# Kernel tuning notes

Hardware: AMD Instinct MI355X
Metric: run time of the kernel (lower is better)

Reference implementation:

```python
import jax, jax.numpy as jnp
import numpy as np

B, S, L = 2, 512, 12
DIM, H, HD = 1024, 16, 64
MAX_SEQ, DFF = 1024, 4096
VOCAB, CODE_HEADS = 2048, 7
THETA, EPS = 10000.0, 1e-5


def _rope_tables():
    inv_freq = 1.0 / (THETA ** (jnp.arange(0, HD, 2, dtype=jnp.float32) / HD))
    t = jnp.arange(MAX_SEQ, dtype=jnp.float32)
    freqs = t[:, None] * inv_freq[None, :]          # [MAX, HD/2]
    emb = jnp.concatenate([freqs, freqs], axis=-1)  # [MAX, HD]
    return jnp.cos(emb), jnp.sin(emb)


def _rotate_half(x):
    x1, x2 = x[..., : HD // 2], x[..., HD // 2:]
    return jnp.concatenate([-x2, x1], axis=-1)


def _rms(x, w):
    v = jnp.mean(x * x, axis=-1, keepdims=True)
    return x * jax.lax.rsqrt(v + EPS) * w


def setup_inputs() -> dict:
    key = jax.random.key(0)
    ks = jax.random.split(key, 12)
    std = 0.02
    rn = lambda k, shp: jax.random.normal(k, shp, jnp.float32) * std
    fused_input2 = jax.random.normal(ks[0], (B, S, DIM), jnp.float32)
    primary_hidden = jax.random.normal(ks[1], (B, S, DIM), jnp.float32)
    position_ids = jnp.broadcast_to(jnp.arange(S), (B, S))
    cache_position = jnp.arange(S)
    # causal additive mask over the full cache length
    allowed = jnp.arange(MAX_SEQ)[None, :] <= cache_position[:, None]  # [S, MAX]
    attn_mask = jnp.broadcast_to(
        jnp.where(allowed, 0.0, -1e9)[None, None], (B, 1, S, MAX_SEQ)
    ).astype(jnp.float32)
    return {
        'fused_input2': fused_input2,
        'primary_hidden': primary_hidden,
        'attn_mask': attn_mask,
        'w_bridge': rn(ks[2], (2 * DIM, DIM)),
        'ln1_w': jnp.ones((L, DIM), jnp.float32),
        'wq': rn(ks[3], (L, DIM, DIM)),
        'wk': rn(ks[4], (L, DIM, DIM)),
        'wv': rn(ks[5], (L, DIM, DIM)),
        'wo': rn(ks[6], (L, DIM, DIM)),
        'ln2_w': jnp.ones((L, DIM), jnp.float32),
        'w_gate': rn(ks[7], (L, DIM, DFF)),
        'w_up': rn(ks[8], (L, DIM, DFF)),
        'w_down': rn(ks[9], (L, DFF, DIM)),
        'norm_w': jnp.ones((DIM,), jnp.float32),
        'w_out': rn(ks[10], (CODE_HEADS, DIM, VOCAB)),
        'position_ids': position_ids,
        'cache_position': cache_position,
    }


def reference(fused_input2, primary_hidden, attn_mask, w_bridge, ln1_w, wq, wk, wv,
              wo, ln2_w, w_gate, w_up, w_down, norm_w, w_out,
              position_ids, cache_position):
    rope_cos, rope_sin = _rope_tables()
    cos = rope_cos[position_ids][:, None]  # [B,1,S,HD]
    sin = rope_sin[position_ids][:, None]
    scale = 1.0 / np.sqrt(HD).astype(np.float32)
    h = jnp.concatenate([fused_input2, primary_hidden], axis=-1) @ w_bridge
    for i in range(L):
        x = _rms(h, ln1_w[i])
        q = (x @ wq[i]).reshape(B, S, H, HD).transpose(0, 2, 1, 3)
        k = (x @ wk[i]).reshape(B, S, H, HD).transpose(0, 2, 1, 3)
        v = (x @ wv[i]).reshape(B, S, H, HD).transpose(0, 2, 1, 3)
        q = q * cos + _rotate_half(q) * sin
        k = k * cos + _rotate_half(k) * sin
        # scatter-style KV-cache write at cache_position
        kc = jnp.zeros((B, H, MAX_SEQ, HD), x.dtype).at[:, :, cache_position, :].set(k)
        vc = jnp.zeros((B, H, MAX_SEQ, HD), x.dtype).at[:, :, cache_position, :].set(v)
        s = jnp.einsum('bhsd,bhtd->bhst', q, kc) * scale + attn_mask
        p = jax.nn.softmax(s.astype(jnp.float32), axis=-1).astype(x.dtype)
        o = jnp.einsum('bhst,bhtd->bhsd', p, vc).transpose(0, 2, 1, 3).reshape(B, S, DIM)
        h = h + o @ wo[i]
        r = h
        x = _rms(h, ln2_w[i])
        h = r + (jax.nn.silu(x @ w_gate[i]) * (x @ w_up[i])) @ w_down[i]
    h = _rms(h, norm_w)
    # [B, code_depth-1, S, VOCAB]
    return jnp.einsum('bsd,kdv->bksv', h, w_out).astype(jnp.float32)
```

## Files before the change

### kernel.cpp

```cpp
#include <hip/hip_runtime.h>

#define NB    2
#define SEQ   512
#define NL    12
#define DIM   1024
#define NH    16
#define HD    64
#define DFF   4096
#define VOCAB 2048
#define CHD   7

typedef __attribute__((ext_vector_type(4))) float f32x4;
typedef __attribute__((ext_vector_type(8))) short s16x8;
typedef __attribute__((ext_vector_type(4))) unsigned short u16x4;
typedef __attribute__((ext_vector_type(8))) unsigned short u16x8;

__device__ __forceinline__ unsigned short f2bf(float f) {
    unsigned u = __builtin_bit_cast(unsigned, f);
    u += 0x7fffu + ((u >> 16) & 1u);
    return (unsigned short)(u >> 16);
}

__device__ __forceinline__ void gl2lds16(const void* g, void* l) {
    __builtin_amdgcn_global_load_lds(
        (const __attribute__((address_space(1))) void*)g,
        (__attribute__((address_space(3))) void*)l, 16, 0, 0);
}

template<bool ATOMIC>
__global__ __launch_bounds__(256)
void gemm_bf(const unsigned short* __restrict__ A,
             const unsigned short* __restrict__ B0,
             const unsigned short* __restrict__ B1,
             const unsigned short* __restrict__ B2,
             float* __restrict__ C, int K, int lda, int ldbT, int ldc,
             int rhi, long sBz, long sCz, int kchunk, int ksplit)
{
    __shared__ unsigned short sm[4][8192];

    const int tid = threadIdx.x;
    const int z   = blockIdx.z;
    const int wsel = z / ksplit, kz = z - wsel * ksplit;
    const int m0  = blockIdx.y * 128;
    const int n0  = blockIdx.x * 128;
    const int koff = kz * kchunk;

    const unsigned short* Ap = A + koff;
    const unsigned short* Bp = sBz ? (B0 + (long)wsel * sBz)
                                   : (wsel == 0 ? B0 : (wsel == 1 ? B1 : B2));
    Bp += koff;
    float* Cp = C + (long)wsel * sCz;

    const int w = tid >> 6, l = tid & 63;
    const int lrow = l & 15, lhi = l >> 4;
    const int wm = (w >> 1) * 64, wn = (w & 1) * 64;

    int rowS[4], colS[4];
    #pragma unroll
    for (int i = 0; i < 4; ++i) {
        const int c = w * 256 + i * 64 + l;
        rowS[i] = c >> 3;
        colS[i] = (((c & 7) ^ ((c >> 3) & 7)) << 3);
    }

    f32x4 acc[4][4] = {};

    auto STAGE = [&](int d, int k0) {
        unsigned short* Ab = &sm[d * 2][0];
        unsigned short* Bb = &sm[d * 2 + 1][0];
        #pragma unroll
        for (int i = 0; i < 4; ++i) {
            const int ub = (w * 256 + i * 64) * 8;
            gl2lds16(Ap + (long)(m0 + rowS[i]) * lda + k0 + colS[i], Ab + ub);
            gl2lds16(Bp + (long)(n0 + rowS[i]) * ldbT + k0 + colS[i], Bb + ub);
        }
    };
    auto COMPUTE = [&](int d) {
        const char* Ab = (const char*)&sm[d * 2][0];
        const char* Bb = (const char*)&sm[d * 2 + 1][0];
        #pragma unroll
        for (int ks = 0; ks < 2; ++ks) {
            s16x8 af[4], bf[4];
            #pragma unroll
            for (int i = 0; i < 4; ++i) {
                const int r = wm + i * 16 + lrow;
                af[i] = __builtin_bit_cast(s16x8, *reinterpret_cast<const u16x8*>(
                    Ab + r * 128 + (((ks * 4 + lhi) ^ (r & 7)) << 4)));
            }
            #pragma unroll
            for (int j = 0; j < 4; ++j) {
                const int r = wn + j * 16 + lrow;
                bf[j] = __builtin_bit_cast(s16x8, *reinterpret_cast<const u16x8*>(
                    Bb + r * 128 + (((ks * 4 + lhi) ^ (r & 7)) << 4)));
            }
            #pragma unroll
            for (int i = 0; i < 4; ++i)
                #pragma unroll
                for (int j = 0; j < 4; ++j)
                    acc[i][j] = __builtin_amdgcn_mfma_f32_16x16x32_bf16(af[i], bf[j], acc[i][j], 0, 0, 0);
        }
    };

    STAGE(0, 0);
    __syncthreads();
    int cur = 0;
    for (int k0 = 0; k0 < K; k0 += 64) {
        if (k0 + 64 < K) STAGE(cur ^ 1, k0 + 64);
        COMPUTE(cur);
        __syncthreads();
        cur ^= 1;
    }

    #pragma unroll
    for (int i = 0; i < 4; ++i) {
        const int r0 = m0 + wm + i * 16 + lhi * 4;
        #pragma unroll
        for (int j = 0; j < 4; ++j) {
            const int c = n0 + wn + j * 16 + lrow;
            #pragma unroll
            for (int e = 0; e < 4; ++e) {
                const int r = r0 + e;
                const long idx = (long)(r >> 9) * rhi + (long)(r & 511) * ldc + c;
                if (ATOMIC) atomicAdd(&Cp[idx], acc[i][j][e]);
                else        Cp[idx] = acc[i][j][e];
            }
        }
    }
}

__global__ __launch_bounds__(256)
void gemm_gu(const unsigned short* __restrict__ A,
             const unsigned short* __restrict__ Bg0,
             const unsigned short* __restrict__ Bu0,
             unsigned short* __restrict__ GU, int K, int lda, int ldbT)
{
    __shared__ unsigned short sm[32768];
    char* const lds = (char*)sm;

    const int tid = threadIdx.x;
    const int m0  = blockIdx.y * 128;
    const int n0  = blockIdx.x * 64;

    const unsigned short* Bg = Bg0 + (long)n0 * ldbT;
    const unsigned short* Bu = Bu0 + (long)n0 * ldbT;

    const int w = tid >> 6, l = tid & 63;
    const int lrow = l & 15, lhi = l >> 4;
    const int wm = (w >> 1) * 64, wn = (w & 1) * 32;

    int rowA[4], colA[4];
    #pragma unroll
    for (int i = 0; i < 4; ++i) {
        const int c = w * 256 + i * 64 + l;
        rowA[i] = c >> 3;
        colA[i] = (((c & 7) ^ ((c >> 3) & 7)) << 3);
    }
    int rowB[2], colB[2];
    #pragma unroll
    for (int i = 0; i < 2; ++i) {
        const int c = w * 128 + i * 64 + l;
        rowB[i] = c >> 3;
        colB[i] = (((c & 7) ^ ((c >> 3) & 7)) << 3);
    }

    f32x4 accg[4][2] = {};
    f32x4 accu[4][2] = {};

    auto STAGE = [&](int d, int k0) {
        char* Ab  = lds + d * 16384;
        char* Bgb = lds + 32768 + d * 8192;
        char* Bub = lds + 49152 + d * 8192;
        #pragma unroll
        for (int i = 0; i < 4; ++i) {
            const int ub = (w * 256 + i * 64) * 16;
            gl2lds16(A + (long)(m0 + rowA[i]) * lda + k0 + colA[i], Ab + ub);
        }
        #pragma unroll
        for (int i = 0; i < 2; ++i) {
            const int ub = (w * 128 + i * 64) * 16;
            gl2lds16(Bg + (long)rowB[i] * ldbT + k0 + colB[i], Bgb + ub);
            gl2lds16(Bu + (long)rowB[i] * ldbT + k0 + colB[i], Bub + ub);
        }
    };
    auto COMPUTE = [&](int d) {
        const char* Ab  = lds + d * 16384;
        const char* Bgb = lds + 32768 + d * 8192;
        const char* Bub = lds + 49152 + d * 8192;
        #pragma unroll
        for (int ks = 0; ks < 2; ++ks) {
            s16x8 af[4], bg[2], bu[2];
            #pragma unroll
            for (int i = 0; i < 4; ++i) {
                const int r = wm + i * 16 + lrow;
                af[i] = __builtin_bit_cast(s16x8, *reinterpret_cast<const u16x8*>(
                    Ab + r * 128 + (((ks * 4 + lhi) ^ (r & 7)) << 4)));
            }
            #pragma unroll
            for (int j = 0; j < 2; ++j) {
                const int r = wn + j * 16 + lrow;
                const int off = r * 128 + (((ks * 4 + lhi) ^ (r & 7)) << 4);
                bg[j] = __builtin_bit_cast(s16x8, *reinterpret_cast<const u16x8*>(Bgb + off));
                bu[j] = __builtin_bit_cast(s16x8, *reinterpret_cast<const u16x8*>(Bub + off));
            }
            #pragma unroll
            for (int i = 0; i < 4; ++i)
                #pragma unroll
                for (int j = 0; j < 2; ++j) {
                    accg[i][j] = __builtin_amdgcn_mfma_f32_16x16x32_bf16(af[i], bg[j], accg[i][j], 0, 0, 0);
                    accu[i][j] = __builtin_amdgcn_mfma_f32_16x16x32_bf16(af[i], bu[j], accu[i][j], 0, 0, 0);
                }
        }
    };

    STAGE(0, 0);
    __syncthreads();
    int cur = 0;
    for (int k0 = 0; k0 < K; k0 += 64) {
        if (k0 + 64 < K) STAGE(cur ^ 1, k0 + 64);
        COMPUTE(cur);
        __syncthreads();
        cur ^= 1;
    }

    #pragma unroll
    for (int i = 0; i < 4; ++i) {
        const int r0 = m0 + wm + i * 16 + lhi * 4;
        #pragma unroll
        for (int j = 0; j < 2; ++j) {
            const int c = n0 + wn + j * 16 + lrow;
            #pragma unroll
            for (int e = 0; e < 4; ++e) {
                const float gx = accg[i][j][e];
                const float ux = accu[i][j][e];
                const float val = gx / (1.0f + __expf(-gx)) * ux;
                GU[(long)(r0 + e) * DFF + c] = f2bf(val);
            }
        }
    }
}

__global__ __launch_bounds__(256)
void tconv_kernel(const float* __restrict__ src, unsigned short* __restrict__ dst,
                  int R, int Cn, long sS, long sD)
{
    __shared__ float tile[64][65];
    const int c0 = blockIdx.x * 64, r0 = blockIdx.y * 64;
    const float* s = src + (long)blockIdx.z * sS;
    unsigned short* d = dst + (long)blockIdx.z * sD;
    const int tid = threadIdx.x;
    #pragma unroll
    for (int it = 0; it < 4; ++it) {
        const int idx = tid + it * 256;
        const int r = idx >> 4, c4 = (idx & 15) * 4;
        f32x4 v = *reinterpret_cast<const f32x4*>(&s[(long)(r0 + r) * Cn + c0 + c4]);
        tile[r][c4] = v[0]; tile[r][c4+1] = v[1]; tile[r][c4+2] = v[2]; tile[r][c4+3] = v[3];
    }
    __syncthreads();
    #pragma unroll
    for (int it = 0; it < 4; ++it) {
        const int idx = tid + it * 256;
        const int n = idx >> 4, r4 = (idx & 15) * 4;
        u16x4 o = { f2bf(tile[r4][n]), f2bf(tile[r4+1][n]),
                    f2bf(tile[r4+2][n]), f2bf(tile[r4+3][n]) };
        *reinterpret_cast<u16x4*>(&d[(long)(c0 + n) * R + r0 + r4]) = o;
    }
}

__global__ __launch_bounds__(256)
void ropetab_kernel(float* __restrict__ tc, float* __restrict__ ts)
{
    const int idx = blockIdx.x * 256 + threadIdx.x;
    const int pos = idx >> 5, i = idx & 31;
    const float invf = powf(10000.0f, -(float)i * (1.0f / 32.0f));
    const float ang = (float)pos * invf;
    tc[idx] = cosf(ang);
    ts[idx] = sinf(ang);
}

template<bool BF>
__global__ __launch_bounds__(256)
void concat_kernel(const float* __restrict__ a, const float* __restrict__ b,
                   void* __restrict__ outv)
{
    const long i = ((long)blockIdx.x * 256 + threadIdx.x) * 4;
    const int row = (int)(i >> 11), col = (int)(i & 2047);
    const float* src = (col < DIM) ? &a[(long)row * DIM + col]
                                   : &b[(long)row * DIM + col - DIM];
    f32x4 v = *reinterpret_cast<const f32x4*>(src);
    if (BF) {
        u16x4 o = { f2bf(v[0]), f2bf(v[1]), f2bf(v[2]), f2bf(v[3]) };
        *reinterpret_cast<u16x4*>((unsigned short*)outv + i) = o;
    } else {
        *reinterpret_cast<f32x4*>((float*)outv + i) = v;
    }
}

template<bool BF>
__global__ __launch_bounds__(256)
void rms_kernel(const float* __restrict__ in, const float* __restrict__ w,
                void* __restrict__ outv)
{
    __shared__ float red[4];
    const int row = blockIdx.x, tid = threadIdx.x;
    const long base = (long)row * DIM + tid * 4;
    f32x4 v = *reinterpret_cast<const f32x4*>(&in[base]);
    float ss = v[0]*v[0] + v[1]*v[1] + v[2]*v[2] + v[3]*v[3];
    for (int off = 32; off; off >>= 1) ss += __shfl_down(ss, off);
    if ((tid & 63) == 0) red[tid >> 6] = ss;
    __syncthreads();
    float s = red[0] + red[1] + red[2] + red[3];
    float r = 1.0f / sqrtf(s * (1.0f / DIM) + 1e-5f);
    f32x4 wv = *reinterpret_cast<const f32x4*>(&w[tid * 4]);
    f32x4 o = { v[0]*r*wv[0], v[1]*r*wv[1], v[2]*r*wv[2], v[3]*r*wv[3] };
    if (BF) {
        u16x4 ob = { f2bf(o[0]), f2bf(o[1]), f2bf(o[2]), f2bf(o[3]) };
        *reinterpret_cast<u16x4*>((unsigned short*)outv + base) = ob;
    } else {
        *reinterpret_cast<f32x4*>((float*)outv + base) = o;
    }
}

template<bool BF>
__global__ __launch_bounds__(256)
void attn_fused(const float* __restrict__ q, const float* __restrict__ k,
                const float* __restrict__ v,
                const float* __restrict__ tc, const float* __restrict__ ts,
                const int* __restrict__ pid, void* __restrict__ attv)
{
    __shared__ unsigned short Qs[64][72];
    __shared__ unsigned short Ps[64][72];
    __shared__ unsigned short Ks[2][64][72];
    __shared__ unsigned short Vs[2][64][72];
    const int tid = threadIdx.x;
    const int qt = blockIdx.x, bh = blockIdx.y, b = bh >> 4, h = bh & 15;
    const int q0 = qt * 64;
    const int w = tid >> 6, l = tid & 63, lrow = l & 15, lhi = l >> 4;

    #pragma unroll
    for (int it = 0; it < 8; ++it) {
        const int idx = tid + it * 256;
        const int r = idx >> 5, i = idx & 31;
        const int tok = b * SEQ + q0 + r;
        const int pos = pid[tok];
        const float c = tc[pos * 32 + i], sn = ts[pos * 32 + i];
        const float* qp = &q[(long)tok * DIM + h * HD];
        const float a1 = qp[i], a2 = qp[i + 32];
        Qs[r][i]      = f2bf(a1 * c - a2 * sn);
        Qs[r][i + 32] = f2bf(a2 * c + a1 * sn);
    }

    auto STAGE_KV = [&](int kt, int d) {
        const int t0 = kt * 64;
        #pragma unroll
        for (int it = 0; it < 8; ++it) {
            const int idx = tid + it * 256;
            const int r = idx >> 5, i = idx & 31;
            const int tok = b * SEQ + t0 + r;
            const int pos = pid[tok];
            const float c = tc[pos * 32 + i], sn = ts[pos * 32 + i];
            const float* kp = &k[(long)tok * DIM + h * HD];
            const float a1 = kp[i], a2 = kp[i + 32];
            Ks[d][r][i]      = f2bf(a1 * c - a2 * sn);
            Ks[d][r][i + 32] = f2bf(a2 * c + a1 * sn);
        }
        #pragma unroll
        for (int it = 0; it < 4; ++it) {
            const int idx = tid + it * 256;
            const int t = idx >> 4, c4 = (idx & 15) * 4;
            f32x4 vv = *reinterpret_cast<const f32x4*>(
                &v[(long)(b * SEQ + t0 + t) * DIM + h * HD + c4]);
            Vs[d][c4][t] = f2bf(vv[0]); Vs[d][c4+1][t] = f2bf(vv[1]);
            Vs[d][c4+2][t] = f2bf(vv[2]); Vs[d][c4+3][t] = f2bf(vv[3]);
        }
    };

    float m_run[4], l_run[4];
    f32x4 o[4] = {};
    #pragma unroll
    for (int j = 0; j < 4; ++j) { m_run[j] = -1e30f; l_run[j] = 0.f; }
    const float scale = 0.125f;

    STAGE_KV(0, 0);
    __syncthreads();

    for (int kt = 0; kt <= qt; ++kt) {
        const int cur = kt & 1;
        const int t0 = kt * 64;
        if (kt < qt) STAGE_KV(kt + 1, cur ^ 1);

        f32x4 s[4] = {};
        #pragma unroll
        for (int ks = 0; ks < 2; ++ks) {
            s16x8 aq = __builtin_bit_cast(s16x8,
                *reinterpret_cast<const u16x8*>(&Qs[w * 16 + lrow][ks * 32 + lhi * 8]));
            #pragma unroll
            for (int j = 0; j < 4; ++j) {
                s16x8 bk = __builtin_bit_cast(s16x8,
                    *reinterpret_cast<const u16x8*>(&Ks[cur][j * 16 + lrow][ks * 32 + lhi * 8]));
                s[j] = __builtin_amdgcn_mfma_f32_16x16x32_bf16(aq, bk, s[j], 0, 0, 0);
            }
        }

        float pv[4][4], corr[4];
        #pragma unroll
        for (int j = 0; j < 4; ++j) {
            const int qrow = q0 + w * 16 + lhi * 4 + j;
            float sv[4], mx = -1e30f;
            #pragma unroll
            for (int tcq = 0; tcq < 4; ++tcq) {
                const int tcur = t0 + tcq * 16 + lrow;
                float vvv = s[tcq][j] * scale;
                if (tcur > qrow) vvv = -1e30f;
                sv[tcq] = vvv;
                mx = fmaxf(mx, vvv);
            }
            #pragma unroll
            for (int mk = 1; mk < 16; mk <<= 1) mx = fmaxf(mx, __shfl_xor(mx, mk));
            const float mnew = fmaxf(m_run[j], mx);
            const float c = __expf(m_run[j] - mnew);
            m_run[j] = mnew;
            float rs = 0.f;
            #pragma unroll
            for (int tcq = 0; tcq < 4; ++tcq) {
                float p = __expf(sv[tcq] - mnew);
                pv[tcq][j] = p;
                rs += p;
            }
            #pragma unroll
            for (int mk = 1; mk < 16; mk <<= 1) rs += __shfl_xor(rs, mk);
            l_run[j] = l_run[j] * c + rs;
            corr[j] = c;
        }

        #pragma unroll
        for (int tcq = 0; tcq < 4; ++tcq)
            #pragma unroll
            for (int j = 0; j < 4; ++j)
                Ps[w * 16 + lhi * 4 + j][tcq * 16 + lrow] = f2bf(pv[tcq][j]);

        #pragma unroll
        for (int dn = 0; dn < 4; ++dn)
            #pragma unroll
            for (int j = 0; j < 4; ++j)
                o[dn][j] *= corr[j];
        #pragma unroll
        for (int ks = 0; ks < 2; ++ks) {
            s16x8 ap = __builtin_bit_cast(s16x8,
                *reinterpret_cast<const u16x8*>(&Ps[w * 16 + lrow][ks * 32 + lhi * 8]));
            #pragma unroll
            for (int dn = 0; dn < 4; ++dn) {
                s16x8 bv = __builtin_bit_cast(s16x8,
                    *reinterpret_cast<const u16x8*>(&Vs[cur][dn * 16 + lrow][ks * 32 + lhi * 8]));
                o[dn] = __builtin_amdgcn_mfma_f32_16x16x32_bf16(ap, bv, o[dn], 0, 0, 0);
            }
        }
        __syncthreads();
    }

    #pragma unroll
    for (int dn = 0; dn < 4; ++dn)
        #pragma unroll
        for (int j = 0; j < 4; ++j) {
            const int qrow = q0 + w * 16 + lhi * 4 + j;
            const int d = dn * 16 + lrow;
            const long idx = (((long)(b * SEQ + qrow)) * NH + h) * HD + d;
            const float val = o[dn][j] / l_run[j];
            if (BF) ((unsigned short*)attv)[idx] = f2bf(val);
            else    ((float*)attv)[idx] = val;
        }
}

__device__ __forceinline__ int swz_b(int row, int col_u16) {
    return row * 128 + ((((col_u16 >> 3) ^ (row & 7)) << 4)) + ((col_u16 << 1) & 15);
}

template<bool ATOMIC, bool SILU>
__global__ __launch_bounds__(256)
void gemm128(const float* __restrict__ A, const float* __restrict__ A2,
             const float* __restrict__ B0, const float* __restrict__ B1,
             const float* __restrict__ B2, float* __restrict__ C,
             int K, int lda, int ldb, int ldc,
             int rhi, long sBz, long sCz, int kchunk)
{
    __shared__ unsigned short As[128 * 64];
    __shared__ unsigned short Bs[128 * 64];
    char* const Ab = reinterpret_cast<char*>(As);
    char* const Bb = reinterpret_cast<char*>(Bs);

    const int tid = threadIdx.x;
    const int z   = blockIdx.z;
    const int m0  = blockIdx.y * 128;
    const int n0  = blockIdx.x * 128;

    const float* Bp = sBz ? (B0 + (long)z * sBz) : (z == 0 ? B0 : (z == 1 ? B1 : B2));
    const long koff = (long)z * kchunk;
    const float* Ap  = A + koff;
    const float* A2p = SILU ? (A2 + koff) : nullptr;
    Bp += koff * (long)ldb;
    float* Cp = C + (long)z * sCz;

    const int w = tid >> 6, l = tid & 63;
    const int lrow = l & 15, lhi = l >> 4;
    const int wm = (w >> 1) * 64, wn = (w & 1) * 64;

    f32x4 acc[4][4] = {};

    for (int k0 = 0; k0 < K; k0 += 64) {
        __syncthreads();
        #pragma unroll
        for (int it = 0; it < 8; ++it) {
            const int idx = tid + it * 256;
            const int m = idx >> 4, c4 = (idx & 15) << 2;
            const long ga = (long)(m0 + m) * lda + k0 + c4;
            float4 v = *reinterpret_cast<const float4*>(&Ap[ga]);
            if (SILU) {
                const float4 v2 = *reinterpret_cast<const float4*>(&A2p[ga]);
                v.x = v.x / (1.0f + __expf(-v.x)) * v2.x;
                v.y = v.y / (1.0f + __expf(-v.y)) * v2.y;
                v.z = v.z / (1.0f + __expf(-v.z)) * v2.z;
                v.w = v.w / (1.0f + __expf(-v.w)) * v2.w;
            }
            u16x4 p = { f2bf(v.x), f2bf(v.y), f2bf(v.z), f2bf(v.w) };
            *reinterpret_cast<u16x4*>(Ab + swz_b(m, c4)) = p;
        }
        #pragma unroll
        for (int it = 0; it < 8; ++it) {
            const int idx = tid + it * 256;
            const int n = idx & 127, kq = idx >> 7;
            const long bb = (long)(k0 + kq * 4) * ldb + n0 + n;
            const float b0v = Bp[bb];
            const float b1v = Bp[bb + ldb];
            const float b2v = Bp[bb + 2 * (long)ldb];
            const float b3v = Bp[bb + 3 * (long)ldb];
            u16x4 p = { f2bf(b0v), f2bf(b1v), f2bf(b2v), f2bf(b3v) };
            *reinterpret_cast<u16x4*>(Bb + swz_b(n, kq << 2)) = p;
        }
        __syncthreads();

        #pragma unroll
        for (int ks = 0; ks < 2; ++ks) {
            s16x8 af[4], bfr[4];
            #pragma unroll
            for (int i = 0; i < 4; ++i) {
                const int r = wm + i * 16 + lrow;
                af[i] = __builtin_bit_cast(s16x8,
                    *reinterpret_cast<const u16x8*>(Ab + swz_b(r, ks * 32 + lhi * 8)));
            }
            #pragma unroll
            for (int j = 0; j < 4; ++j) {
                const int r = wn + j * 16 + lrow;
                bfr[j] = __builtin_bit_cast(s16x8,
                    *reinterpret_cast<const u16x8*>(Bb + swz_b(r, ks * 32 + lhi * 8)));
            }
            #pragma unroll
            for (int i = 0; i < 4; ++i)
                #pragma unroll
                for (int j = 0; j < 4; ++j)
                    acc[i][j] = __builtin_amdgcn_mfma_f32_16x16x32_bf16(af[i], bfr[j], acc[i][j], 0, 0, 0);
        }
    }

    #pragma unroll
    for (int i = 0; i < 4; ++i) {
        const int r0 = m0 + wm + i * 16 + lhi * 4;
        #pragma unroll
        for (int j = 0; j < 4; ++j) {
            const int c = n0 + wn + j * 16 + lrow;
            #pragma unroll
            for (int e = 0; e < 4; ++e) {
                const int r = r0 + e;
                const long idx = (long)(r >> 9) * rhi + (long)(r & 511) * ldc + c;
                if (ATOMIC) atomicAdd(&Cp[idx], acc[i][j][e]);
                else        Cp[idx] = acc[i][j][e];
            }
        }
    }
}

__global__ __launch_bounds__(256)
void rope_kernel(float* __restrict__ q, float* __restrict__ k,
                 const int* __restrict__ pid)
{
    const int t = blockIdx.x * 256 + threadIdx.x;
    const int i = t & 31, h = (t >> 5) & 15, s = (t >> 9) & 511, b = t >> 18;
    const int pos = pid[b * SEQ + s];
    const float invf = powf(10000.0f, -(float)i * (1.0f / 32.0f));
    const float ang = (float)pos * invf;
    const float c = cosf(ang), sn = sinf(ang);
    const long base = (((long)(b * SEQ + s)) * NH + h) * HD + i;
    float a1 = q[base], a2 = q[base + 32];
    q[base] = a1 * c - a2 * sn;  q[base + 32] = a2 * c + a1 * sn;
    float b1 = k[base], b2 = k[base + 32];
    k[base] = b1 * c - b2 * sn;  k[base + 32] = b2 * c + b1 * sn;
}

__global__ __launch_bounds__(256)
void transpose_v_kernel(const float* __restrict__ v, float* __restrict__ vT)
{
    __shared__ float tile[64][65];
    const int st = blockIdx.x, bh = blockIdx.y, b = bh >> 4, h = bh & 15;
    const int s0 = st * 64;
    for (int t = threadIdx.x; t < 64 * 16; t += 256) {
        int s = t >> 4, c4 = (t & 15) * 4;
        f32x4 v4 = *reinterpret_cast<const f32x4*>(
            &v[(((long)(b * SEQ + s0 + s)) * NH + h) * HD + c4]);
        tile[s][c4] = v4[0]; tile[s][c4+1] = v4[1]; tile[s][c4+2] = v4[2]; tile[s][c4+3] = v4[3];
    }
    __syncthreads();
    for (int t = threadIdx.x; t < 64 * 16; t += 256) {
        int d = t >> 4, c4 = (t & 15) * 4;
        f32x4 o4 = { tile[c4][d], tile[c4+1][d], tile[c4+2][d], tile[c4+3][d] };
        *reinterpret_cast<f32x4*>(&vT[((long)bh * HD + d) * SEQ + s0 + c4]) = o4;
    }
}

template<bool BF>
__global__ __launch_bounds__(256)
void attn_kernel(const float* __restrict__ q, const float* __restrict__ k,
                 const float* __restrict__ vT, void* __restrict__ attv)
{
    __shared__ unsigned short Qs[64][72];
    __shared__ unsigned short Ks[64][72];
    __shared__ unsigned short Ps[64][72];
    __shared__ unsigned short Vs[64][72];
    const int tid = threadIdx.x;
    const int qt = blockIdx.x, bh = blockIdx.y, b = bh >> 4, h = bh & 15;
    const int q0 = qt * 64;
    const int w = tid >> 6, l = tid & 63, lrow = l & 15, lhi = l >> 4;

    for (int t = tid; t < 64 * 16; t += 256) {
        int r = t >> 4, c4 = (t & 15) * 4;
        f32x4 v4 = *reinterpret_cast<const f32x4*>(
            &q[(((long)(b * SEQ + q0 + r)) * NH + h) * HD + c4]);
        u16x4 p = { f2bf(v4[0]), f2bf(v4[1]), f2bf(v4[2]), f2bf(v4[3]) };
        *reinterpret_cast<u16x4*>(&Qs[r][c4]) = p;
    }

    float m_run[4], l_run[4];
    f32x4 o[4] = {};
    #pragma unroll
    for (int j = 0; j < 4; ++j) { m_run[j] = -1e30f; l_run[j] = 0.f; }
    const float scale = 0.125f;

    for (int kt = 0; kt <= qt; ++kt) {
        const int t0 = kt * 64;
        __syncthreads();
        for (int t = tid; t < 64 * 16; t += 256) {
            int r = t >> 4, c4 = (t & 15) * 4;
            f32x4 v4 = *reinterpret_cast<const f32x4*>(
                &k[(((long)(b * SEQ + t0 + r)) * NH + h) * HD + c4]);
            u16x4 p = { f2bf(v4[0]), f2bf(v4[1]), f2bf(v4[2]), f2bf(v4[3]) };
            *reinterpret_cast<u16x4*>(&Ks[r][c4]) = p;
        }
        for (int t = tid; t < 64 * 16; t += 256) {
            int d = t >> 4, c4 = (t & 15) * 4;
            f32x4 v4 = *reinterpret_cast<const f32x4*>(
                &vT[((long)bh * HD + d) * SEQ + t0 + c4]);
            u16x4 p = { f2bf(v4[0]), f2bf(v4[1]), f2bf(v4[2]), f2bf(v4[3]) };
            *reinterpret_cast<u16x4*>(&Vs[d][c4]) = p;
        }
        __syncthreads();

        f32x4 s[4] = {};
        #pragma unroll
        for (int ks = 0; ks < 2; ++ks) {
            s16x8 aq = __builtin_bit_cast(s16x8,
                *reinterpret_cast<const u16x8*>(&Qs[w * 16 + lrow][ks * 32 + lhi * 8]));
            #pragma unroll
            for (int j = 0; j < 4; ++j) {
                s16x8 bk = __builtin_bit_cast(s16x8,
                    *reinterpret_cast<const u16x8*>(&Ks[j * 16 + lrow][ks * 32 + lhi * 8]));
                s[j] = __builtin_amdgcn_mfma_f32_16x16x32_bf16(aq, bk, s[j], 0, 0, 0);
            }
        }

        float pv[4][4], corr[4];
        #pragma unroll
        for (int j = 0; j < 4; ++j) {
            const int qrow = q0 + w * 16 + lhi * 4 + j;
            float sv[4], mx = -1e30f;
            #pragma unroll
            for (int tcq = 0; tcq < 4; ++tcq) {
                const int tcur = t0 + tcq * 16 + lrow;
                float vvv = s[tcq][j] * scale;
                if (tcur > qrow) vvv = -1e30f;
                sv[tcq] = vvv;
                mx = fmaxf(mx, vvv);
            }
            #pragma unroll
            for (int mk = 1; mk < 16; mk <<= 1) mx = fmaxf(mx, __shfl_xor(mx, mk));
            const float mnew = fmaxf(m_run[j], mx);
            const float c = __expf(m_run[j] - mnew);
            m_run[j] = mnew;
            float rs = 0.f;
            #pragma unroll
            for (int tcq = 0; tcq < 4; ++tcq) {
                float p = __expf(sv[tcq] - mnew);
                pv[tcq][j] = p;
                rs += p;
            }
            #pragma unroll
            for (int mk = 1; mk < 16; mk <<= 1) rs += __shfl_xor(rs, mk);
            l_run[j] = l_run[j] * c + rs;
            corr[j] = c;
        }

        #pragma unroll
        for (int tcq = 0; tcq < 4; ++tcq)
            #pragma unroll
            for (int j = 0; j < 4; ++j)
                Ps[w * 16 + lhi * 4 + j][tcq * 16 + lrow] = f2bf(pv[tcq][j]);

        #pragma unroll
        for (int dn = 0; dn < 4; ++dn)
            #pragma unroll
            for (int j = 0; j < 4; ++j)
                o[dn][j] *= corr[j];
        #pragma unroll
        for (int ks = 0; ks < 2; ++ks) {
            s16x8 ap = __builtin_bit_cast(s16x8,
                *reinterpret_cast<const u16x8*>(&Ps[w * 16 + lrow][ks * 32 + lhi * 8]));
            #pragma unroll
            for (int dn = 0; dn < 4; ++dn) {
                s16x8 bv = __builtin_bit_cast(s16x8,
                    *reinterpret_cast<const u16x8*>(&Vs[dn * 16 + lrow][ks * 32 + lhi * 8]));
                o[dn] = __builtin_amdgcn_mfma_f32_16x16x32_bf16(ap, bv, o[dn], 0, 0, 0);
            }
        }
    }

    #pragma unroll
    for (int dn = 0; dn < 4; ++dn)
        #pragma unroll
        for (int j = 0; j < 4; ++j) {
            const int qrow = q0 + w * 16 + lhi * 4 + j;
            const int d = dn * 16 + lrow;
            const long idx = (((long)(b * SEQ + qrow)) * NH + h) * HD + d;
            const float val = o[dn][j] / l_run[j];
            if (BF) ((unsigned short*)attv)[idx] = f2bf(val);
            else    ((float*)attv)[idx] = val;
        }
}

__global__ __launch_bounds__(256)
void silu_bf_kernel(const float* __restrict__ g, const float* __restrict__ u,
                    unsigned short* __restrict__ o)
{
    const long i = ((long)blockIdx.x * 256 + threadIdx.x) * 4;
    f32x4 gv = *reinterpret_cast<const f32x4*>(&g[i]);
    f32x4 uv = *reinterpret_cast<const f32x4*>(&u[i]);
    u16x4 r;
    #pragma unroll
    for (int e = 0; e < 4; ++e) {
        float gx = gv[e];
        r[e] = f2bf(gx / (1.0f + __expf(-gx)) * uv[e]);
    }
    *reinterpret_cast<u16x4*>(&o[i]) = r;
}

extern "C" void kernel_launch(void* const* d_in, const int* in_sizes, int n_in,
                              void* d_out, int out_size, void* d_ws, size_t ws_size,
                              hipStream_t stream)
{
    const float* f2   = (const float*)d_in[0];
    const float* ph   = (const float*)d_in[1];
    const float* wbr  = (const float*)d_in[3];
    const float* ln1  = (const float*)d_in[4];
    const float* wq   = (const float*)d_in[5];
    const float* wk   = (const float*)d_in[6];
    const float* wv   = (const float*)d_in[7];
    const float* wo   = (const float*)d_in[8];
    const float* ln2  = (const float*)d_in[9];
    const float* wg   = (const float*)d_in[10];
    const float* wu   = (const float*)d_in[11];
    const float* wd   = (const float*)d_in[12];
    const float* nw   = (const float*)d_in[13];
    const float* wout = (const float*)d_in[14];
    const int*   pid  = (const int*)d_in[15];
    float* out = (float*)d_out;

    const long M1 = 1048576;
    dim3 blk(256);

    const size_t NEED = (size_t)122 * M1 * 4;
    if (ws_size >= NEED) {
        float* ws = (float*)d_ws;
        float* h    = ws;
        float* q    = ws + 1 * M1;
        float* k    = ws + 2 * M1;
        float* v    = ws + 3 * M1;
        float* tcos = ws + 12 * M1;
        float* tsin = ws + 12 * M1 + 16384;
        unsigned short* xcat_bf = (unsigned short*)(ws + 13 * M1);
        unsigned short* x_bf    = (unsigned short*)(ws + 14 * M1);
        unsigned short* att_bf  = (unsigned short*)(ws + 14 * M1 + 524288);
        unsigned short* gu_bf   = (unsigned short*)(ws + 15 * M1);
        unsigned short* wT      = (unsigned short*)(ws + 17 * M1);
        unsigned short* wbrT  = wT;
        unsigned short* wqT   = wbrT + 2 * M1;
        unsigned short* wkT   = wqT + 12 * M1;
        unsigned short* wvT   = wkT + 12 * M1;
        unsigned short* woT   = wvT + 12 * M1;
        unsigned short* wgT   = woT + 12 * M1;
        unsigned short* wuT   = wgT + 48 * M1;
        unsigned short* wdT   = wuT + 48 * M1;
        unsigned short* woutT = wdT + 48 * M1;

        ropetab_kernel<<<64, blk, 0, stream>>>(tcos, tsin);
        tconv_kernel<<<dim3(16, 32, 1), blk, 0, stream>>>(wbr, wbrT, 2048, 1024, 0, 0);
        tconv_kernel<<<dim3(16, 16, NL), blk, 0, stream>>>(wq, wqT, 1024, 1024, M1, M1);
        tconv_kernel<<<dim3(16, 16, NL), blk, 0, stream>>>(wk, wkT, 1024, 1024, M1, M1);
        tconv_kernel<<<dim3(16, 16, NL), blk, 0, stream>>>(wv, wvT, 1024, 1024, M1, M1);
        tconv_kernel<<<dim3(16, 16, NL), blk, 0, stream>>>(wo, woT, 1024, 1024, M1, M1);
        tconv_kernel<<<dim3(64, 16, NL), blk, 0, stream>>>(wg, wgT, 1024, 4096, 4 * M1, 4 * M1);
        tconv_kernel<<<dim3(64, 16, NL), blk, 0, stream>>>(wu, wuT, 1024, 4096, 4 * M1, 4 * M1);
        tconv_kernel<<<dim3(16, 64, NL), blk, 0, stream>>>(wd, wdT, 4096, 1024, 4 * M1, 4 * M1);
        tconv_kernel<<<dim3(32, 16, CHD), blk, 0, stream>>>(wout, woutT, 1024, 2048, 2 * M1, 2 * M1);

        concat_kernel<true><<<2048, blk, 0, stream>>>(f2, ph, xcat_bf);
        hipMemsetAsync(h, 0, M1 * 4, stream);
        gemm_bf<true><<<dim3(8, 8, 4), blk, 0, stream>>>(
            xcat_bf, wbrT, wbrT, wbrT, h, 512, 2048, 2048, 1024, 512 * 1024, 0, 0, 512, 4);

        for (int i = 0; i < NL; ++i) {
            rms_kernel<true><<<1024, blk, 0, stream>>>(h, ln1 + (long)i * DIM, x_bf);
            gemm_bf<false><<<dim3(8, 8, 3), blk, 0, stream>>>(
                x_bf, wqT + (long)i * M1, wkT + (long)i * M1, wvT + (long)i * M1, q,
                1024, 1024, 1024, 1024, 512 * 1024, 0, M1, 0, 1);
            attn_fused<true><<<dim3(8, 32), blk, 0, stream>>>(
                q, k, v, tcos, tsin, pid, att_bf);
            gemm_bf<true><<<dim3(8, 8, 4), blk, 0, stream>>>(
                att_bf, woT + (long)i * M1, woT + (long)i * M1, woT + (long)i * M1, h,
                256, 1024, 1024, 1024, 512 * 1024, 0, 0, 256, 4);

            rms_kernel<true><<<1024, blk, 0, stream>>>(h, ln2 + (long)i * DIM, x_bf);
            gemm_gu<<<dim3(64, 8), blk, 0, stream>>>(
                x_bf, wgT + (long)i * 4 * M1, wuT + (long)i * 4 * M1, gu_bf, 1024, 1024, 1024);
            gemm_bf<true><<<dim3(8, 8, 8), blk, 0, stream>>>(
                gu_bf, wdT + (long)i * 4 * M1, wdT + (long)i * 4 * M1, wdT + (long)i * 4 * M1, h,
                512, 4096, 4096, 1024, 512 * 1024, 0, 0, 512, 8);
        }

        rms_kernel<true><<<1024, blk, 0, stream>>>(h, nw, x_bf);
        gemm_bf<false><<<dim3(16, 8, CHD), blk, 0, stream>>>(
            x_bf, woutT, nullptr, nullptr, out,
            1024, 1024, 1024, 2048, CHD * 512 * 2048, 2 * M1, (long)512 * 2048, 0, 1);
        return;
    }

    float* ws = (float*)d_ws;
    float* xcat = ws;
    float* h    = ws + 2 * M1;
    float* x    = ws + 3 * M1;
    float* q    = ws + 4 * M1;
    float* kb   = ws + 5 * M1;
    float* v    = ws + 6 * M1;
    float* vT   = ws + 7 * M1;
    float* att  = ws + 8 * M1;
    float* g    = ws + 9 * M1;
    float* u    = ws + 13 * M1;

    concat_kernel<false><<<2048, blk, 0, stream>>>(f2, ph, xcat);
    gemm128<false, false><<<dim3(8, 8, 1), blk, 0, stream>>>(
        xcat, nullptr, wbr, wbr, wbr, h, 2048, 2048, DIM, DIM, 512 * DIM, 0, 0, 0);

    for (int i = 0; i < NL; ++i) {
        rms_kernel<false><<<1024, blk, 0, stream>>>(h, ln1 + (long)i * DIM, x);
        gemm128<false, false><<<dim3(8, 8, 3), blk, 0, stream>>>(
            x, nullptr, wq + (long)i * M1, wk + (long)i * M1, wv + (long)i * M1, q,
            1024, DIM, DIM, DIM, 512 * DIM, 0, M1, 0);
        rope_kernel<<<2048, blk, 0, stream>>>(q, kb, pid);
        transpose_v_kernel<<<dim3(8, 32), blk, 0, stream>>>(v, vT);
        attn_kernel<false><<<dim3(8, 32), blk, 0, stream>>>(q, kb, vT, att);
        gemm128<true, false><<<dim3(8, 8, 2), blk, 0, stream>>>(
            att, nullptr, wo + (long)i * M1, wo + (long)i * M1, wo + (long)i * M1, h,
            512, DIM, DIM, DIM, 512 * DIM, 0, 0, 512);

        rms_kernel<false><<<1024, blk, 0, stream>>>(h, ln2 + (long)i * DIM, x);
        gemm128<false, false><<<dim3(32, 8, 1), blk, 0, stream>>>(
            x, nullptr, wg + (long)i * 4 * M1, wg + (long)i * 4 * M1, wg + (long)i * 4 * M1, g,
            1024, DIM, DFF, DFF, 512 * DFF, 0, 0, 0);
        gemm128<false, false><<<dim3(32, 8, 1), blk, 0, stream>>>(
            x, nullptr, wu + (long)i * 4 * M1, wu + (long)i * 4 * M1, wu + (long)i * 4 * M1, u,
            1024, DIM, DFF, DFF, 512 * DFF, 0, 0, 0);
        gemm128<true, true><<<dim3(8, 8, 4), blk, 0, stream>>>(
            g, u, wd + (long)i * 4 * M1, wd + (long)i * 4 * M1, wd + (long)i * 4 * M1, h,
            1024, DFF, DIM, DIM, 512 * DIM, 0, 0, 1024);
    }

    rms_kernel<false><<<1024, blk, 0, stream>>>(h, nw, x);
    gemm128<false, false><<<dim3(16, 8, CHD), blk, 0, stream>>>(
        x, nullptr, wout, wout, wout, out,
        1024, DIM, VOCAB, VOCAB, CHD * 512 * VOCAB, (long)DIM * VOCAB, (long)512 * VOCAB, 0);
}
```

Baseline: 1.852 ms.

## Fuse RoPE and bf16 conversion into QKV GEMM epilogue, async-load attention tiles

The QKV projection GEMM now applies rotary embedding to Q and K and writes bf16 outputs directly, with V stored transposed per head. The attention kernel then stages Q/K/V tiles with direct global-to-LDS loads into XOR-swizzled shared memory instead of reading fp32 and rotating/converting per tile. It also raises wave priority around the MFMA blocks. This removes fp32 intermediate traffic and redundant RoPE work on K, which was recomputed by every query tile. The cost is scattered 2-byte stores in the GEMM epilogue, particularly the transposed V writes.

```diff
diff --git a/kernel.cpp b/kernel.cpp
--- a/kernel.cpp
+++ b/kernel.cpp
@@ -27,14 +27,16 @@
         (__attribute__((address_space(3))) void*)l, 16, 0, 0);
 }
 
-template<bool ATOMIC>
+template<int EPI>
 __global__ __launch_bounds__(256)
 void gemm_bf(const unsigned short* __restrict__ A,
              const unsigned short* __restrict__ B0,
              const unsigned short* __restrict__ B1,
              const unsigned short* __restrict__ B2,
              float* __restrict__ C, int K, int lda, int ldbT, int ldc,
-             int rhi, long sBz, long sCz, int kchunk, int ksplit)
+             int rhi, long sBz, long sCz, int kchunk, int ksplit,
+             const float* __restrict__ tc, const float* __restrict__ ts,
+             const int* __restrict__ pid, unsigned short* __restrict__ qkv_bf)
 {
     __shared__ unsigned short sm[4][8192];
 
@@ -111,6 +113,40 @@
         cur ^= 1;
     }
 
+    if (EPI == 2) {
+        const int h = (n0 + wn) >> 6;
+        unsigned short* qb = qkv_bf;
+        unsigned short* kb = qkv_bf + 1048576;
+        unsigned short* vt = qkv_bf + 2097152;
+        #pragma unroll
+        for (int i = 0; i < 4; ++i) {
+            const int r0 = m0 + wm + i * 16 + lhi * 4;
+            #pragma unroll
+            for (int e = 0; e < 4; ++e) {
+                const int r = r0 + e;
+                if (wsel == 2) {
+                    const int bh = (r >> 9) * NH + h, s = r & 511;
+                    #pragma unroll
+                    for (int j = 0; j < 4; ++j)
+                        vt[((long)(bh * 64 + j * 16 + lrow)) * 512 + s] = f2bf(acc[i][j][e]);
+                } else {
+                    unsigned short* ob = (wsel == 0) ? qb : kb;
+                    const int pos = pid[r];
+                    const float c0 = tc[pos * 32 + lrow],      s0 = ts[pos * 32 + lrow];
+                    const float c1 = tc[pos * 32 + 16 + lrow], s1 = ts[pos * 32 + 16 + lrow];
+                    const float a0 = acc[i][0][e], a1 = acc[i][1][e];
+                    const float a2 = acc[i][2][e], a3 = acc[i][3][e];
+                    const long rb = (long)r * DIM + (n0 + wn) + lrow;
+                    ob[rb]      = f2bf(a0 * c0 - a2 * s0);
+                    ob[rb + 16] = f2bf(a1 * c1 - a3 * s1);
+                    ob[rb + 32] = f2bf(a2 * c0 + a0 * s0);
+                    ob[rb + 48] = f2bf(a3 * c1 + a1 * s1);
+                }
+            }
+        }
+        return;
+    }
+
     #pragma unroll
     for (int i = 0; i < 4; ++i) {
         const int r0 = m0 + wm + i * 16 + lhi * 4;
@@ -121,8 +157,8 @@
             for (int e = 0; e < 4; ++e) {
                 const int r = r0 + e;
                 const long idx = (long)(r >> 9) * rhi + (long)(r & 511) * ldc + c;
-                if (ATOMIC) atomicAdd(&Cp[idx], acc[i][j][e]);
-                else        Cp[idx] = acc[i][j][e];
+                if (EPI == 1) atomicAdd(&Cp[idx], acc[i][j][e]);
+                else          Cp[idx] = acc[i][j][e];
             }
         }
     }
@@ -320,58 +356,42 @@
     }
 }
 
-template<bool BF>
-__global__ __launch_bounds__(256)
-void attn_fused(const float* __restrict__ q, const float* __restrict__ k,
-                const float* __restrict__ v,
-                const float* __restrict__ tc, const float* __restrict__ ts,
-                const int* __restrict__ pid, void* __restrict__ attv)
-{
-    __shared__ unsigned short Qs[64][72];
+__global__ __launch_bounds__(256)
+void attn_bf(const unsigned short* __restrict__ qb,
+             const unsigned short* __restrict__ kb,
+             const unsigned short* __restrict__ vt,
+             unsigned short* __restrict__ attv)
+{
+    __shared__ unsigned short Qs[4096];
     __shared__ unsigned short Ps[64][72];
-    __shared__ unsigned short Ks[2][64][72];
-    __shared__ unsigned short Vs[2][64][72];
+    __shared__ unsigned short Ks[2][4096];
+    __shared__ unsigned short Vs[2][4096];
     const int tid = threadIdx.x;
     const int qt = blockIdx.x, bh = blockIdx.y, b = bh >> 4, h = bh & 15;
     const int q0 = qt * 64;
     const int w = tid >> 6, l = tid & 63, lrow = l & 15, lhi = l >> 4;
 
-    #pragma unroll
-    for (int it = 0; it < 8; ++it) {
-        const int idx = tid + it * 256;
-        const int r = idx >> 5, i = idx & 31;
-        const int tok = b * SEQ + q0 + r;
-        const int pos = pid[tok];
-        const float c = tc[pos * 32 + i], sn = ts[pos * 32 + i];
-        const float* qp = &q[(long)tok * DIM + h * HD];
-        const float a1 = qp[i], a2 = qp[i + 32];
-        Qs[r][i]      = f2bf(a1 * c - a2 * sn);
-        Qs[r][i + 32] = f2bf(a2 * c + a1 * sn);
-    }
+    int rowS[2], colS[2];
+    #pragma unroll
+    for (int i = 0; i < 2; ++i) {
+        const int c = w * 128 + i * 64 + l;
+        rowS[i] = c >> 3;
+        colS[i] = (((c & 7) ^ ((c >> 3) & 7)) << 3);
+    }
+
+    auto STAGE64 = [&](const unsigned short* src, long rstride, unsigned short* dst) {
+        #pragma unroll
+        for (int i = 0; i < 2; ++i)
+            gl2lds16(src + (long)rowS[i] * rstride + colS[i],
+                     dst + (w * 128 + i * 64) * 8);
+    };
+
+    STAGE64(qb + (long)(b * SEQ + q0) * DIM + h * HD, DIM, Qs);
 
     auto STAGE_KV = [&](int kt, int d) {
         const int t0 = kt * 64;
-        #pragma unroll
-        for (int it = 0; it < 8; ++it) {
-            const int idx = tid + it * 256;
-            const int r = idx >> 5, i = idx & 31;
-            const int tok = b * SEQ + t0 + r;
-            const int pos = pid[tok];
-            const float c = tc[pos * 32 + i], sn = ts[pos * 32 + i];
-            const float* kp = &k[(long)tok * DIM + h * HD];
-            const float a1 = kp[i], a2 = kp[i + 32];
-            Ks[d][r][i]      = f2bf(a1 * c - a2 * sn);
-            Ks[d][r][i + 32] = f2bf(a2 * c + a1 * sn);
-        }
-        #pragma unroll
-        for (int it = 0; it < 4; ++it) {
-            const int idx = tid + it * 256;
-            const int t = idx >> 4, c4 = (idx & 15) * 4;
-            f32x4 vv = *reinterpret_cast<const f32x4*>(
-                &v[(long)(b * SEQ + t0 + t) * DIM + h * HD + c4]);
-            Vs[d][c4][t] = f2bf(vv[0]); Vs[d][c4+1][t] = f2bf(vv[1]);
-            Vs[d][c4+2][t] = f2bf(vv[2]); Vs[d][c4+3][t] = f2bf(vv[3]);
-        }
+        STAGE64(kb + (long)(b * SEQ + t0) * DIM + h * HD, DIM, Ks[d]);
+        STAGE64(vt + (long)(bh * 64) * 512 + t0, 512, Vs[d]);
     };
 
     float m_run[4], l_run[4];
@@ -389,17 +409,21 @@
         if (kt < qt) STAGE_KV(kt + 1, cur ^ 1);
 
         f32x4 s[4] = {};
+        __builtin_amdgcn_s_setprio(1);
         #pragma unroll
         for (int ks = 0; ks < 2; ++ks) {
-            s16x8 aq = __builtin_bit_cast(s16x8,
-                *reinterpret_cast<const u16x8*>(&Qs[w * 16 + lrow][ks * 32 + lhi * 8]));
+            const int rq = w * 16 + lrow;
+            s16x8 aq = __builtin_bit_cast(s16x8, *reinterpret_cast<const u16x8*>(
+                (const char*)Qs + rq * 128 + (((ks * 4 + lhi) ^ (rq & 7)) << 4)));
             #pragma unroll
             for (int j = 0; j < 4; ++j) {
-                s16x8 bk = __builtin_bit_cast(s16x8,
-                    *reinterpret_cast<const u16x8*>(&Ks[cur][j * 16 + lrow][ks * 32 + lhi * 8]));
+                const int rk = j * 16 + lrow;
+                s16x8 bk = __builtin_bit_cast(s16x8, *reinterpret_cast<const u16x8*>(
+                    (const char*)Ks[cur] + rk * 128 + (((ks * 4 + lhi) ^ (rk & 7)) << 4)));
                 s[j] = __builtin_amdgcn_mfma_f32_16x16x32_bf16(aq, bk, s[j], 0, 0, 0);
             }
         }
+        __builtin_amdgcn_s_setprio(0);
 
         float pv[4][4], corr[4];
         #pragma unroll
@@ -443,17 +467,20 @@
             #pragma unroll
             for (int j = 0; j < 4; ++j)
                 o[dn][j] *= corr[j];
+        __builtin_amdgcn_s_setprio(1);
         #pragma unroll
         for (int ks = 0; ks < 2; ++ks) {
             s16x8 ap = __builtin_bit_cast(s16x8,
                 *reinterpret_cast<const u16x8*>(&Ps[w * 16 + lrow][ks * 32 + lhi * 8]));
             #pragma unroll
             for (int dn = 0; dn < 4; ++dn) {
-                s16x8 bv = __builtin_bit_cast(s16x8,
-                    *reinterpret_cast<const u16x8*>(&Vs[cur][dn * 16 + lrow][ks * 32 + lhi * 8]));
+                const int rv = dn * 16 + lrow;
+                s16x8 bv = __builtin_bit_cast(s16x8, *reinterpret_cast<const u16x8*>(
+                    (const char*)Vs[cur] + rv * 128 + (((ks * 4 + lhi) ^ (rv & 7)) << 4)));
                 o[dn] = __builtin_amdgcn_mfma_f32_16x16x32_bf16(ap, bv, o[dn], 0, 0, 0);
             }
         }
+        __builtin_amdgcn_s_setprio(0);
         __syncthreads();
     }
 
@@ -464,9 +491,7 @@
             const int qrow = q0 + w * 16 + lhi * 4 + j;
             const int d = dn * 16 + lrow;
             const long idx = (((long)(b * SEQ + qrow)) * NH + h) * HD + d;
-            const float val = o[dn][j] / l_run[j];
-            if (BF) ((unsigned short*)attv)[idx] = f2bf(val);
-            else    ((float*)attv)[idx] = val;
+            attv[idx] = f2bf(o[dn][j] / l_run[j]);
         }
 }
 
@@ -786,15 +811,13 @@
     if (ws_size >= NEED) {
         float* ws = (float*)d_ws;
         float* h    = ws;
-        float* q    = ws + 1 * M1;
-        float* k    = ws + 2 * M1;
-        float* v    = ws + 3 * M1;
-        float* tcos = ws + 12 * M1;
-        float* tsin = ws + 12 * M1 + 16384;
-        unsigned short* xcat_bf = (unsigned short*)(ws + 13 * M1);
-        unsigned short* x_bf    = (unsigned short*)(ws + 14 * M1);
-        unsigned short* att_bf  = (unsigned short*)(ws + 14 * M1 + 524288);
-        unsigned short* gu_bf   = (unsigned short*)(ws + 15 * M1);
+        float* tcos = ws + 1 * M1;
+        float* tsin = ws + 1 * M1 + 16384;
+        unsigned short* xcat_bf = (unsigned short*)(ws + 2 * M1);
+        unsigned short* x_bf    = (unsigned short*)(ws + 3 * M1);
+        unsigned short* att_bf  = (unsigned short*)(ws + 3 * M1 + 524288);
+        unsigned short* gu_bf   = (unsigned short*)(ws + 4 * M1);
+        unsigned short* qkv_bf  = (unsigned short*)(ws + 6 * M1);
         unsigned short* wT      = (unsigned short*)(ws + 17 * M1);
         unsigned short* wbrT  = wT;
         unsigned short* wqT   = wbrT + 2 * M1;
@@ -819,32 +842,37 @@
 
         concat_kernel<true><<<2048, blk, 0, stream>>>(f2, ph, xcat_bf);
         hipMemsetAsync(h, 0, M1 * 4, stream);
-        gemm_bf<true><<<dim3(8, 8, 4), blk, 0, stream>>>(
-            xcat_bf, wbrT, wbrT, wbrT, h, 512, 2048, 2048, 1024, 512 * 1024, 0, 0, 512, 4);
+        gemm_bf<1><<<dim3(8, 8, 4), blk, 0, stream>>>(
+            xcat_bf, wbrT, wbrT, wbrT, h, 512, 2048, 2048, 1024, 512 * 1024, 0, 0, 512, 4,
+            nullptr, nullptr, nullptr, nullptr);
 
         for (int i = 0; i < NL; ++i) {
             rms_kernel<true><<<1024, blk, 0, stream>>>(h, ln1 + (long)i * DIM, x_bf);
-            gemm_bf<false><<<dim3(8, 8, 3), blk, 0, stream>>>(
-                x_bf, wqT + (long)i * M1, wkT + (long)i * M1, wvT + (long)i * M1, q,
-                1024, 1024, 1024, 1024, 512 * 1024, 0, M1, 0, 1);
-            attn_fused<true><<<dim3(8, 32), blk, 0, stream>>>(
-                q, k, v, tcos, tsin, pid, att_bf);
-            gemm_bf<true><<<dim3(8, 8, 4), blk, 0, stream>>>(
+            gemm_bf<2><<<dim3(8, 8, 3), blk, 0, stream>>>(
+                x_bf, wqT + (long)i * M1, wkT + (long)i * M1, wvT + (long)i * M1, nullptr,
+                1024, 1024, 1024, 1024, 0, 0, 0, 0, 1,
+                tcos, tsin, pid, qkv_bf);
+            attn_bf<<<dim3(8, 32), blk, 0, stream>>>(
+                qkv_bf, qkv_bf + M1, qkv_bf + 2 * M1, att_bf);
+            gemm_bf<1><<<dim3(8, 8, 4), blk, 0, stream>>>(
                 att_bf, woT + (long)i * M1, woT + (long)i * M1, woT + (long)i * M1, h,
-                256, 1024, 1024, 1024, 512 * 1024, 0, 0, 256, 4);
+                256, 1024, 1024, 1024, 512 * 1024, 0, 0, 256, 4,
+                nullptr, nullptr, nullptr, nullptr);
 
             rms_kernel<true><<<1024, blk, 0, stream>>>(h, ln2 + (long)i * DIM, x_bf);
             gemm_gu<<<dim3(64, 8), blk, 0, stream>>>(
                 x_bf, wgT + (long)i * 4 * M1, wuT + (long)i * 4 * M1, gu_bf, 1024, 1024, 1024);
-            gemm_bf<true><<<dim3(8, 8, 8), blk, 0, stream>>>(
+            gemm_bf<1><<<dim3(8, 8, 8), blk, 0, stream>>>(
                 gu_bf, wdT + (long)i * 4 * M1, wdT + (long)i * 4 * M1, wdT + (long)i * 4 * M1, h,
-                512, 4096, 4096, 1024, 512 * 1024, 0, 0, 512, 8);
+                512, 4096, 4096, 1024, 512 * 1024, 0, 0, 512, 8,
+                nullptr, nullptr, nullptr, nullptr);
         }
 
         rms_kernel<true><<<1024, blk, 0, stream>>>(h, nw, x_bf);
-        gemm_bf<false><<<dim3(16, 8, CHD), blk, 0, stream>>>(
+        gemm_bf<0><<<dim3(16, 8, CHD), blk, 0, stream>>>(
             x_bf, woutT, nullptr, nullptr, out,
-            1024, 1024, 1024, 2048, CHD * 512 * 2048, 2 * M1, (long)512 * 2048, 0, 1);
+            1024, 1024, 1024, 2048, CHD * 512 * 2048, 2 * M1, (long)512 * 2048, 0, 1,
+            nullptr, nullptr, nullptr, nullptr);
         return;
     }
 
```

Result: no change. 1.847 ms (-0.3%).
